# Optimization experiments

Measured on AMD Instinct MI355X. Metric: run time of the kernel, lower is better.

The kernel has to match this reference:

```python
import jax, jax.numpy as jnp
import numpy as np

N_NODES = 100000
N_EDGES = 1600000
D = 128
N_LAYERS = 3
N_GRAPHS = 64
BN_EPS = 1e-5


def setup_inputs() -> dict:
    key = jax.random.key(0)
    ks = jax.random.split(key, 8)
    x = jax.random.normal(ks[0], (N_NODES, D), dtype=jnp.float32)
    edge_index = jax.random.randint(ks[1], (2, N_EDGES), 0, N_NODES, dtype=jnp.int64)
    batch = jnp.sort(jax.random.randint(ks[2], (N_NODES,), 0, N_GRAPHS, dtype=jnp.int64))
    scale = 1.0 / np.sqrt(D)
    W1 = jax.random.normal(ks[3], (N_LAYERS, D, D), dtype=jnp.float32) * scale
    W2 = jax.random.normal(ks[4], (N_LAYERS, D, D), dtype=jnp.float32) * scale
    g1 = jnp.ones((N_LAYERS, D), dtype=jnp.float32)
    b1 = jnp.zeros((N_LAYERS, D), dtype=jnp.float32)
    g2 = jnp.ones((N_LAYERS, D), dtype=jnp.float32)
    b2 = jnp.zeros((N_LAYERS, D), dtype=jnp.float32)
    eps = jnp.zeros((N_LAYERS,), dtype=jnp.float32)
    return {"x": x, "edge_index": edge_index, "batch": batch,
            "W1": W1, "g1": g1, "b1": b1, "W2": W2, "g2": g2, "b2": b2, "eps": eps}


def _batchnorm(z, gamma, beta):
    # BatchNorm1d in training mode: biased variance over the node dimension.
    mu = jnp.mean(z, axis=0, keepdims=True)
    var = jnp.mean(jnp.square(z - mu), axis=0, keepdims=True)
    return (z - mu) * jax.lax.rsqrt(var + BN_EPS) * gamma + beta


def reference(x, edge_index, batch, W1, g1, b1, W2, g2, b2, eps):
    src, dst = edge_index[0], edge_index[1]
    h = x
    for l in range(N_LAYERS):
        # GIN aggregation: sum of neighbor features via edge-index scatter-add
        agg = jax.ops.segment_sum(h[src], dst, num_segments=N_NODES)
        z = (1.0 + eps[l]) * h + agg
        # MLP: Linear(no bias) -> BN -> ReLU -> Linear(no bias) -> BN
        z = _batchnorm(z @ W1[l], g1[l], b1[l])
        z = jax.nn.relu(z)
        z = _batchnorm(z @ W2[l], g2[l], b2[l])
        h = jax.nn.relu(z)  # gnn_non_linear
    node_emb = h
    # mean readout per graph
    counts = jax.ops.segment_sum(jnp.ones((N_NODES,), dtype=h.dtype), batch, num_segments=N_GRAPHS)
    graph_sum = jax.ops.segment_sum(h, batch, num_segments=N_GRAPHS)
    graph_emb = graph_sum / jnp.maximum(counts, 1.0)[:, None]
    # emb_normalize -> F.normalize(p=2, dim=-1)
    graph_emb = graph_emb / jnp.maximum(jnp.linalg.norm(graph_emb, axis=-1, keepdims=True), 1e-12)
    return node_emb, graph_emb
```

## Files before the change

### kernel.cpp

```cpp
#include <hip/hip_runtime.h>

#define N_NODES 100000
#define N_EDGES 1600000
#define D 128
#define N_GRAPHS 64
#define BN_EPS 1e-5f
#define NSLICE 16

#define BNODES 256
#define NBUCK ((N_NODES + BNODES - 1) / BNODES)
#define EPB 8192
#define NABLK ((N_EDGES + EPB - 1) / EPB)

typedef short short8 __attribute__((ext_vector_type(8)));
typedef float f32x4 __attribute__((ext_vector_type(4)));

__device__ inline unsigned short f2bf(float f) {
  unsigned int u = __float_as_uint(f);
  u += 0x7fffu + ((u >> 16) & 1);
  return (unsigned short)(u >> 16);
}
__device__ inline float bf2f(unsigned short h) {
  return __uint_as_float(((unsigned int)h) << 16);
}
__device__ inline void unpack8(uint4 u, float* f) {
  f[0] = __uint_as_float(u.x << 16); f[1] = __uint_as_float(u.x & 0xffff0000u);
  f[2] = __uint_as_float(u.y << 16); f[3] = __uint_as_float(u.y & 0xffff0000u);
  f[4] = __uint_as_float(u.z << 16); f[5] = __uint_as_float(u.z & 0xffff0000u);
  f[6] = __uint_as_float(u.w << 16); f[7] = __uint_as_float(u.w & 0xffff0000u);
}
__device__ inline uint4 pack8(const float* f) {
  uint4 u;
  u.x = f2bf(f[0]) | ((unsigned)f2bf(f[1]) << 16);
  u.y = f2bf(f[2]) | ((unsigned)f2bf(f[3]) << 16);
  u.z = f2bf(f[4]) | ((unsigned)f2bf(f[5]) << 16);
  u.w = f2bf(f[6]) | ((unsigned)f2bf(f[7]) << 16);
  return u;
}

__global__ __launch_bounds__(256) void k_cast(const float* __restrict__ in,
                                              unsigned short* __restrict__ o) {
  long i = ((long)blockIdx.x * blockDim.x + threadIdx.x) * 8;
  if (i >= (long)N_NODES * D) return;
  float4 a = *(const float4*)(in + i);
  float4 b = *(const float4*)(in + i + 4);
  float f[8] = {a.x, a.y, a.z, a.w, b.x, b.y, b.z, b.w};
  *(uint4*)(o + i) = pack8(f);
}

__global__ __launch_bounds__(128) void k_wprep(const float* __restrict__ W1,
                                               const float* __restrict__ W2,
                                               unsigned short* __restrict__ Wt) {
  int m = blockIdx.x;
  int n = blockIdx.y;
  int k = threadIdx.x;
  int l = m >> 1, s = m & 1;
  const float* W = (s == 0 ? W1 : W2) + (size_t)l * D * D;
  Wt[((size_t)m * D + n) * D + k] = f2bf(W[(size_t)k * D + n]);
}

__global__ __launch_bounds__(256) void k_histb(const int* __restrict__ dst,
                                               int* __restrict__ ecount) {
  __shared__ int lh[NBUCK];
  const int t = threadIdx.x;
  const int e0 = blockIdx.x * EPB;
  const int e1 = min(e0 + EPB, N_EDGES);
  for (int i = t; i < NBUCK; i += 256) lh[i] = 0;
  __syncthreads();
  for (int e = e0 + t; e < e1; e += 256) atomicAdd(&lh[dst[e] >> 8], 1);
  __syncthreads();
  for (int i = t; i < NBUCK; i += 256)
    if (lh[i]) atomicAdd(&ecount[i], lh[i]);
}

__global__ __launch_bounds__(512) void k_scanb(const int* __restrict__ ecount,
                                               int* __restrict__ ebase,
                                               int* __restrict__ gcur) {
  __shared__ int ls[512];
  int t = threadIdx.x;
  int v = (t < NBUCK) ? ecount[t] : 0;
  ls[t] = v;
  __syncthreads();
  for (int o = 1; o < 512; o <<= 1) {
    int u = (t >= o) ? ls[t - o] : 0;
    __syncthreads();
    ls[t] += u;
    __syncthreads();
  }
  int ex = ls[t] - v;
  if (t < NBUCK) { ebase[t] = ex; gcur[t] = ex; }
  if (t == 0) ebase[NBUCK] = N_EDGES;
}

__global__ __launch_bounds__(256) void k_scatA(const int* __restrict__ ei,
                                               int* __restrict__ gcur,
                                               int2* __restrict__ pairs) {
  __shared__ int lh[NBUCK];
  __shared__ int lbase[NBUCK];
  const int t = threadIdx.x;
  const int e0 = blockIdx.x * EPB;
  const int e1 = min(e0 + EPB, N_EDGES);
  for (int i = t; i < NBUCK; i += 256) lh[i] = 0;
  __syncthreads();
  for (int e = e0 + t; e < e1; e += 256) atomicAdd(&lh[ei[N_EDGES + e] >> 8], 1);
  __syncthreads();
  for (int i = t; i < NBUCK; i += 256)
    lbase[i] = (lh[i] > 0) ? atomicAdd(&gcur[i], lh[i]) : 0;
  __syncthreads();
  for (int e = e0 + t; e < e1; e += 256) {
    int s = ei[e];
    int d = ei[N_EDGES + e];
    int p = atomicAdd(&lbase[d >> 8], 1);
    pairs[p] = make_int2(s, d);
  }
}

__global__ __launch_bounds__(256) void k_scatB(const int2* __restrict__ pairs,
                                               const int* __restrict__ ebase,
                                               int* __restrict__ off,
                                               int* __restrict__ esrc) {
  __shared__ int lcnt[BNODES];
  __shared__ int ls[256];
  const int t = threadIdx.x;
  const int b = blockIdx.x;
  const int nb0 = b * BNODES;
  const int nn = min(BNODES, N_NODES - nb0);
  const int s0 = ebase[b], s1 = ebase[b + 1];
  if (t < nn) lcnt[t] = 0;
  __syncthreads();
  for (int e = s0 + t; e < s1; e += 256) atomicAdd(&lcnt[pairs[e].y - nb0], 1);
  __syncthreads();
  int c0 = (t < nn) ? lcnt[t] : 0;
  ls[t] = c0;
  __syncthreads();
  for (int o = 1; o < 256; o <<= 1) {
    int u = (t >= o) ? ls[t - o] : 0;
    __syncthreads();
    ls[t] += u;
    __syncthreads();
  }
  int pre = ls[t] - c0;
  if (t < nn) {
    off[nb0 + t] = s0 + pre;
    lcnt[t] = s0 + pre;
  }
  __syncthreads();
  for (int e = s0 + t; e < s1; e += 256) {
    int2 p = pairs[e];
    int pos = atomicAdd(&lcnt[p.y - nb0], 1);
    esrc[pos] = p.x;
  }
  if (b == 0 && t == 0) off[N_NODES] = N_EDGES;
}

template <int MODE>
__global__ __launch_bounds__(256) void k_aggz(const unsigned short* __restrict__ h,
                                              const int* __restrict__ off,
                                              const int* __restrict__ esrc,
                                              const float* __restrict__ epsp,
                                              const float* __restrict__ sc,
                                              const float* __restrict__ tb,
                                              unsigned short* __restrict__ z) {
  const int lane = threadIdx.x & 63;
  const int n = blockIdx.x * 4 + (threadIdx.x >> 6);
  const int c = lane << 1;
  float S0 = 0.f, S1 = 0.f, T0 = 0.f, T1 = 0.f;
  if (MODE == 1) { S0 = sc[c]; S1 = sc[c + 1]; T0 = tb[c]; T1 = tb[c + 1]; }
  const float e = 1.0f + epsp[0];
  const int o0 = off[n], o1 = off[n + 1];

  float a0, a1;
  {
    unsigned int u = *(const unsigned int*)(h + (size_t)n * D + c);
    float lo = __uint_as_float(u << 16);
    float hi = __uint_as_float(u & 0xffff0000u);
    if (MODE == 1) {
      lo = fmaxf(fmaf(lo, S0, T0), 0.f);
      hi = fmaxf(fmaf(hi, S1, T1), 0.f);
    }
    a0 = e * lo;
    a1 = e * hi;
  }

  int j = o0;
  for (; j + 7 < o1; j += 8) {
    int i0 = esrc[j], i1 = esrc[j + 1], i2 = esrc[j + 2], i3 = esrc[j + 3];
    int i4 = esrc[j + 4], i5 = esrc[j + 5], i6 = esrc[j + 6], i7 = esrc[j + 7];
    unsigned int u0 = *(const unsigned int*)(h + (size_t)i0 * D + c);
    unsigned int u1 = *(const unsigned int*)(h + (size_t)i1 * D + c);
    unsigned int u2 = *(const unsigned int*)(h + (size_t)i2 * D + c);
    unsigned int u3 = *(const unsigned int*)(h + (size_t)i3 * D + c);
    unsigned int u4 = *(const unsigned int*)(h + (size_t)i4 * D + c);
    unsigned int u5 = *(const unsigned int*)(h + (size_t)i5 * D + c);
    unsigned int u6 = *(const unsigned int*)(h + (size_t)i6 * D + c);
    unsigned int u7 = *(const unsigned int*)(h + (size_t)i7 * D + c);
    float l0 = __uint_as_float(u0 << 16), h0 = __uint_as_float(u0 & 0xffff0000u);
    float l1 = __uint_as_float(u1 << 16), h1 = __uint_as_float(u1 & 0xffff0000u);
    float l2 = __uint_as_float(u2 << 16), h2 = __uint_as_float(u2 & 0xffff0000u);
    float l3 = __uint_as_float(u3 << 16), h3 = __uint_as_float(u3 & 0xffff0000u);
    float l4 = __uint_as_float(u4 << 16), h4 = __uint_as_float(u4 & 0xffff0000u);
    float l5 = __uint_as_float(u5 << 16), h5 = __uint_as_float(u5 & 0xffff0000u);
    float l6 = __uint_as_float(u6 << 16), h6 = __uint_as_float(u6 & 0xffff0000u);
    float l7 = __uint_as_float(u7 << 16), h7 = __uint_as_float(u7 & 0xffff0000u);
    if (MODE == 1) {
      l0 = fmaxf(fmaf(l0, S0, T0), 0.f); h0 = fmaxf(fmaf(h0, S1, T1), 0.f);
      l1 = fmaxf(fmaf(l1, S0, T0), 0.f); h1 = fmaxf(fmaf(h1, S1, T1), 0.f);
      l2 = fmaxf(fmaf(l2, S0, T0), 0.f); h2 = fmaxf(fmaf(h2, S1, T1), 0.f);
      l3 = fmaxf(fmaf(l3, S0, T0), 0.f); h3 = fmaxf(fmaf(h3, S1, T1), 0.f);
      l4 = fmaxf(fmaf(l4, S0, T0), 0.f); h4 = fmaxf(fmaf(h4, S1, T1), 0.f);
      l5 = fmaxf(fmaf(l5, S0, T0), 0.f); h5 = fmaxf(fmaf(h5, S1, T1), 0.f);
      l6 = fmaxf(fmaf(l6, S0, T0), 0.f); h6 = fmaxf(fmaf(h6, S1, T1), 0.f);
      l7 = fmaxf(fmaf(l7, S0, T0), 0.f); h7 = fmaxf(fmaf(h7, S1, T1), 0.f);
    }
    a0 += ((l0 + l1) + (l2 + l3)) + ((l4 + l5) + (l6 + l7));
    a1 += ((h0 + h1) + (h2 + h3)) + ((h4 + h5) + (h6 + h7));
  }
  for (; j + 3 < o1; j += 4) {
    int i0 = esrc[j], i1 = esrc[j + 1], i2 = esrc[j + 2], i3 = esrc[j + 3];
    unsigned int u0 = *(const unsigned int*)(h + (size_t)i0 * D + c);
    unsigned int u1 = *(const unsigned int*)(h + (size_t)i1 * D + c);
    unsigned int u2 = *(const unsigned int*)(h + (size_t)i2 * D + c);
    unsigned int u3 = *(const unsigned int*)(h + (size_t)i3 * D + c);
    float l0 = __uint_as_float(u0 << 16), h0 = __uint_as_float(u0 & 0xffff0000u);
    float l1 = __uint_as_float(u1 << 16), h1 = __uint_as_float(u1 & 0xffff0000u);
    float l2 = __uint_as_float(u2 << 16), h2 = __uint_as_float(u2 & 0xffff0000u);
    float l3 = __uint_as_float(u3 << 16), h3 = __uint_as_float(u3 & 0xffff0000u);
    if (MODE == 1) {
      l0 = fmaxf(fmaf(l0, S0, T0), 0.f); h0 = fmaxf(fmaf(h0, S1, T1), 0.f);
      l1 = fmaxf(fmaf(l1, S0, T0), 0.f); h1 = fmaxf(fmaf(h1, S1, T1), 0.f);
      l2 = fmaxf(fmaf(l2, S0, T0), 0.f); h2 = fmaxf(fmaf(h2, S1, T1), 0.f);
      l3 = fmaxf(fmaf(l3, S0, T0), 0.f); h3 = fmaxf(fmaf(h3, S1, T1), 0.f);
    }
    a0 += (l0 + l1) + (l2 + l3);
    a1 += (h0 + h1) + (h2 + h3);
  }
  for (; j < o1; j++) {
    unsigned int u0 = *(const unsigned int*)(h + (size_t)esrc[j] * D + c);
    float l0 = __uint_as_float(u0 << 16), h0 = __uint_as_float(u0 & 0xffff0000u);
    if (MODE == 1) {
      l0 = fmaxf(fmaf(l0, S0, T0), 0.f);
      h0 = fmaxf(fmaf(h0, S1, T1), 0.f);
    }
    a0 += l0;
    a1 += h0;
  }
  unsigned int pk = (unsigned int)f2bf(a0) | ((unsigned int)f2bf(a1) << 16);
  *(unsigned int*)(z + (size_t)n * D + c) = pk;
}

template <int MODE>
__global__ __launch_bounds__(256) void k_gemm(const unsigned short* __restrict__ A,
                                              const unsigned short* __restrict__ Wt,
                                              unsigned short* __restrict__ out,
                                              const float* __restrict__ psA,
                                              const float* __restrict__ pqA,
                                              const float* __restrict__ gamA,
                                              const float* __restrict__ betA,
                                              float* __restrict__ ssum,
                                              float* __restrict__ ssq) {
  __shared__ unsigned short Zs[64 * 136];
  __shared__ float psumL[4 * 128];
  __shared__ float psqL[4 * 128];
  __shared__ float scL[128];
  __shared__ float tbL[128];
  const int t = threadIdx.x;
  const int row0 = blockIdx.x * 64;

  if constexpr (MODE == 1) {
    if (t < 128) {
      float S = 0.f, Q = 0.f;
#pragma unroll
      for (int i = 0; i < NSLICE; i++) { S += psA[i * 128 + t]; Q += pqA[i * 128 + t]; }
      float m = S * (1.0f / (float)N_NODES);
      float v = Q * (1.0f / (float)N_NODES) - m * m;
      float r = rsqrtf(v + BN_EPS);
      float s = r * gamA[t];
      scL[t] = s;
      tbL[t] = betA[t] - m * s;
    }
    __syncthreads();
  }

#pragma unroll
  for (int i = 0; i < 4; i++) {
    int q = t + i * 256;
    int r = q >> 4, cb = (q & 15) << 3;
    int grow = row0 + r;
    uint4 u = make_uint4(0u, 0u, 0u, 0u);
    if (grow < N_NODES) {
      u = *(const uint4*)(A + (size_t)grow * D + cb);
      if constexpr (MODE == 1) {
        float f[8];
        unpack8(u, f);
#pragma unroll
        for (int jj = 0; jj < 8; jj++)
          f[jj] = fmaxf(fmaf(f[jj], scL[cb + jj], tbL[cb + jj]), 0.f);
        u = pack8(f);
      }
    }
    *(uint4*)&Zs[r * 136 + cb] = u;
  }
  __syncthreads();

  const int lane = t & 63;
  const int wave = t >> 6;
  const int quad = lane >> 4;
  const int lr = lane & 15;
  const int m0 = wave * 16;

  f32x4 acc[8];
#pragma unroll
  for (int i = 0; i < 8; i++) acc[i] = (f32x4){0.f, 0.f, 0.f, 0.f};

#pragma unroll
  for (int kc = 0; kc < 128; kc += 32) {
    short8 af = *(const short8*)&Zs[(m0 + lr) * 136 + kc + quad * 8];
#pragma unroll
    for (int nt = 0; nt < 8; nt++) {
      short8 bf = *(const short8*)(Wt + (size_t)(nt * 16 + lr) * D + kc + quad * 8);
      acc[nt] = __builtin_amdgcn_mfma_f32_16x16x32_bf16(af, bf, acc[nt], 0, 0, 0);
    }
  }

#pragma unroll
  for (int nt = 0; nt < 8; nt++) {
    float s = acc[nt][0] + acc[nt][1] + acc[nt][2] + acc[nt][3];
    float qq = acc[nt][0] * acc[nt][0] + acc[nt][1] * acc[nt][1] +
               acc[nt][2] * acc[nt][2] + acc[nt][3] * acc[nt][3];
    s += __shfl_xor(s, 16);
    s += __shfl_xor(s, 32);
    qq += __shfl_xor(qq, 16);
    qq += __shfl_xor(qq, 32);
    if (quad == 0) {
      psumL[wave * 128 + nt * 16 + lr] = s;
      psqL[wave * 128 + nt * 16 + lr] = qq;
    }
  }

#pragma unroll
  for (int rr = 0; rr < 4; rr++) {
    int grow = row0 + m0 + quad * 4 + rr;
    if (grow < N_NODES) {
#pragma unroll
      for (int nt = 0; nt < 8; nt++)
        out[(size_t)grow * D + nt * 16 + lr] = f2bf(acc[nt][rr]);
    }
  }

  __syncthreads();
  if (t < 128) {
    float S = psumL[t] + psumL[128 + t] + psumL[256 + t] + psumL[384 + t];
    float Q = psqL[t] + psqL[128 + t] + psqL[256 + t] + psqL[384 + t];
    int slice = blockIdx.x & (NSLICE - 1);
    atomicAdd(&ssum[slice * 128 + t], S);
    atomicAdd(&ssq[slice * 128 + t], Q);
  }
}

__global__ void k_bnfin(const float* __restrict__ ssum, const float* __restrict__ ssq,
                        const float* __restrict__ gamma, const float* __restrict__ beta,
                        float* __restrict__ sc, float* __restrict__ tb) {
  int f = threadIdx.x;
  float S = 0.f, Q = 0.f;
  for (int i = 0; i < NSLICE; i++) { S += ssum[i * 128 + f]; Q += ssq[i * 128 + f]; }
  float m = S * (1.0f / (float)N_NODES);
  float v = Q * (1.0f / (float)N_NODES) - m * m;
  float r = rsqrtf(v + BN_EPS);
  float s = r * gamma[f];
  sc[f] = s;
  tb[f] = beta[f] - m * s;
}

#define RCH 64
__global__ __launch_bounds__(128) void k_readout(const unsigned short* __restrict__ y,
                                                 const int* __restrict__ batch,
                                                 const float* __restrict__ psA,
                                                 const float* __restrict__ pqA,
                                                 const float* __restrict__ gam,
                                                 const float* __restrict__ bet,
                                                 float* __restrict__ node_out,
                                                 float* __restrict__ gsum,
                                                 int* __restrict__ gcnt) {
  int start = blockIdx.x * RCH;
  int end = min(start + RCH, N_NODES);
  if (start >= end) return;
  int f = threadIdx.x;
  float S = 0.f, Q = 0.f;
#pragma unroll
  for (int i = 0; i < NSLICE; i++) { S += psA[i * 128 + f]; Q += pqA[i * 128 + f]; }
  float m = S * (1.0f / (float)N_NODES);
  float v = Q * (1.0f / (float)N_NODES) - m * m;
  float r = rsqrtf(v + BN_EPS);
  float s = r * gam[f];
  float tt = bet[f] - m * s;

  float acc = 0.f;
  int cnt = 0;
  int curg = batch[start];
  for (int n = start; n < end; n++) {
    int gg = batch[n];
    float vv = fmaxf(fmaf(bf2f(y[(size_t)n * D + f]), s, tt), 0.f);
    node_out[(size_t)n * D + f] = vv;
    if (gg != curg) {
      atomicAdd(&gsum[curg * D + f], acc);
      if (f == 0) atomicAdd(&gcnt[curg], cnt);
      acc = 0.f; cnt = 0; curg = gg;
    }
    acc += vv;
    cnt++;
  }
  atomicAdd(&gsum[curg * D + f], acc);
  if (f == 0) atomicAdd(&gcnt[curg], cnt);
}

__global__ __launch_bounds__(128) void k_gnorm(const float* __restrict__ gsum,
                                               const int* __restrict__ gcnt,
                                               float* __restrict__ out) {
  __shared__ float red[128];
  int g = blockIdx.x, f = threadIdx.x;
  float c = (float)gcnt[g];
  float v = gsum[g * D + f] / fmaxf(c, 1.0f);
  red[f] = v * v;
  __syncthreads();
  for (int o = 64; o > 0; o >>= 1) {
    if (f < o) red[f] += red[f + o];
    __syncthreads();
  }
  float nrm = sqrtf(red[0]);
  out[(size_t)g * D + f] = v / fmaxf(nrm, 1e-12f);
}

extern "C" void kernel_launch(void* const* d_in, const int* in_sizes, int n_in,
                              void* d_out, int out_size, void* d_ws, size_t ws_size,
                              hipStream_t stream) {
  const float* x   = (const float*)d_in[0];
  const int*   ei  = (const int*)d_in[1];
  const int*   bat = (const int*)d_in[2];
  const float* W1  = (const float*)d_in[3];
  const float* g1  = (const float*)d_in[4];
  const float* b1  = (const float*)d_in[5];
  const float* W2  = (const float*)d_in[6];
  const float* g2  = (const float*)d_in[7];
  const float* b2  = (const float*)d_in[8];
  const float* eps = (const float*)d_in[9];
  float* out = (float*)d_out;

  char* w = (char*)d_ws;
  const size_t FEAT_B = (size_t)N_NODES * D * 2;
  unsigned short* xb   = (unsigned short*)w; w += FEAT_B;
  unsigned short* bufA = (unsigned short*)w; w += FEAT_B;
  unsigned short* bufB = (unsigned short*)w; w += FEAT_B;
  unsigned short* bufC = (unsigned short*)w; w += FEAT_B;
  unsigned short* WtB  = (unsigned short*)w; w += (size_t)6 * D * D * 2;
  int* off   = (int*)w; w += 400016;
  int* ebase = (int*)w; w += 2048;
  int* gcur  = (int*)w; w += 2048;
  int* esrc  = (int*)w; w += (size_t)N_EDGES * 4;
  float* sc2 = (float*)w; w += 512;
  float* tb2 = (float*)w; w += 512;
  char* zreg = w;
  int* ecount  = (int*)w; w += 2048;
  float* stats = (float*)w; w += (size_t)6 * 2 * NSLICE * 128 * 4;
  float* gsum  = (float*)w; w += (size_t)N_GRAPHS * D * 4;
  int* gcnt    = (int*)w; w += 256;
  size_t zbytes = (size_t)((char*)w - zreg);
  int2* pairs = (int2*)bufA;

  hipMemsetAsync(zreg, 0, zbytes, stream);

  k_cast<<<(N_NODES * D / 8 + 255) / 256, 256, 0, stream>>>(x, xb);
  k_wprep<<<dim3(6, 128), 128, 0, stream>>>(W1, W2, WtB);

  k_histb<<<NABLK, 256, 0, stream>>>(ei + N_EDGES, ecount);
  k_scanb<<<1, 512, 0, stream>>>(ecount, ebase, gcur);
  k_scatA<<<NABLK, 256, 0, stream>>>(ei, gcur, pairs);
  k_scatB<<<NBUCK, 256, 0, stream>>>(pairs, ebase, off, esrc);

  const int gemm_grid = (N_NODES + 63) / 64;
  const int aggz_grid = N_NODES / 4;

  for (int l = 0; l < 3; l++) {
    float* s1 = stats + (size_t)(l * 2 + 0) * 2 * NSLICE * 128;
    float* q1 = s1 + NSLICE * 128;
    float* s2 = stats + (size_t)(l * 2 + 1) * 2 * NSLICE * 128;
    float* q2 = s2 + NSLICE * 128;
    const unsigned short* Wa = WtB + (size_t)(l * 2 + 0) * D * D;
    const unsigned short* Wb = WtB + (size_t)(l * 2 + 1) * D * D;
    if (l == 0) {
      k_aggz<0><<<aggz_grid, 256, 0, stream>>>(xb, off, esrc, eps + l,
                                               nullptr, nullptr, bufA);
    } else {
      k_aggz<1><<<aggz_grid, 256, 0, stream>>>(bufC, off, esrc, eps + l,
                                               sc2, tb2, bufA);
    }
    k_gemm<0><<<gemm_grid, 256, 0, stream>>>(bufA, Wa, bufB,
                                             nullptr, nullptr, nullptr, nullptr,
                                             s1, q1);
    k_gemm<1><<<gemm_grid, 256, 0, stream>>>(bufB, Wb, bufC,
                                             s1, q1, g1 + (size_t)l * D, b1 + (size_t)l * D,
                                             s2, q2);
    if (l < 2) {
      k_bnfin<<<1, 128, 0, stream>>>(s2, q2, g2 + (size_t)l * D, b2 + (size_t)l * D,
                                     sc2, tb2);
    }
  }

  float* ps2f = stats + (size_t)(2 * 2 + 1) * 2 * NSLICE * 128;
  float* pq2f = ps2f + NSLICE * 128;
  k_readout<<<(N_NODES + RCH - 1) / RCH, 128, 0, stream>>>(
      bufC, bat, ps2f, pq2f, g2 + (size_t)2 * D, b2 + (size_t)2 * D,
      out, gsum, gcnt);
  k_gnorm<<<N_GRAPHS, 128, 0, stream>>>(gsum, gcnt, out + (size_t)N_NODES * D);
}
```

Baseline: 644.5 us.

## Split neighbor gather across half-waves with 8-byte loads and fuse BN finalize

```diff
diff --git a/kernel.cpp b/kernel.cpp
--- a/kernel.cpp
+++ b/kernel.cpp
@@ -148,7 +148,7 @@
   for (int e = s0 + t; e < s1; e += 256) {
     int2 p = pairs[e];
     int pos = atomicAdd(&lcnt[p.y - nb0], 1);
-    esrc[pos] = p.x;
+    esrc[pos] = p.x << 8;
   }
   if (b == 0 && t == 0) off[N_NODES] = N_EDGES;
 }
@@ -156,96 +156,99 @@
 template <int MODE>
 __global__ __launch_bounds__(256) void k_aggz(const unsigned short* __restrict__ h,
                                               const int* __restrict__ off,
-                                              const int* __restrict__ esrc,
+                                              const int* __restrict__ esrcB,
                                               const float* __restrict__ epsp,
                                               const float* __restrict__ sc,
                                               const float* __restrict__ tb,
                                               unsigned short* __restrict__ z) {
   const int lane = threadIdx.x & 63;
   const int n = blockIdx.x * 4 + (threadIdx.x >> 6);
-  const int c = lane << 1;
-  float S0 = 0.f, S1 = 0.f, T0 = 0.f, T1 = 0.f;
-  if (MODE == 1) { S0 = sc[c]; S1 = sc[c + 1]; T0 = tb[c]; T1 = tb[c + 1]; }
+  const int half = lane >> 5;
+  const int hl = lane & 31;
+  const int c = hl << 2;
+  const char* hb = (const char*)h;
+  const int cb = hl << 3;
+
+  float S0 = 0.f, S1 = 0.f, S2 = 0.f, S3 = 0.f;
+  float T0 = 0.f, T1 = 0.f, T2 = 0.f, T3 = 0.f;
+  if (MODE == 1) {
+    float4 s4 = *(const float4*)(sc + c);
+    float4 t4 = *(const float4*)(tb + c);
+    S0 = s4.x; S1 = s4.y; S2 = s4.z; S3 = s4.w;
+    T0 = t4.x; T1 = t4.y; T2 = t4.z; T3 = t4.w;
+  }
   const float e = 1.0f + epsp[0];
   const int o0 = off[n], o1 = off[n + 1];
 
-  float a0, a1;
+  float a0, a1, a2, a3;
   {
-    unsigned int u = *(const unsigned int*)(h + (size_t)n * D + c);
-    float lo = __uint_as_float(u << 16);
-    float hi = __uint_as_float(u & 0xffff0000u);
+    uint2 u = *(const uint2*)(hb + (size_t)n * 256 + cb);
+    float v0 = __uint_as_float(u.x << 16), v1 = __uint_as_float(u.x & 0xffff0000u);
+    float v2 = __uint_as_float(u.y << 16), v3 = __uint_as_float(u.y & 0xffff0000u);
     if (MODE == 1) {
-      lo = fmaxf(fmaf(lo, S0, T0), 0.f);
-      hi = fmaxf(fmaf(hi, S1, T1), 0.f);
-    }
-    a0 = e * lo;
-    a1 = e * hi;
+      v0 = fmaxf(fmaf(v0, S0, T0), 0.f); v1 = fmaxf(fmaf(v1, S1, T1), 0.f);
+      v2 = fmaxf(fmaf(v2, S2, T2), 0.f); v3 = fmaxf(fmaf(v3, S3, T3), 0.f);
+    }
+    float ee = (half == 0) ? e : 0.f;
+    a0 = ee * v0; a1 = ee * v1; a2 = ee * v2; a3 = ee * v3;
   }
 
   int j = o0;
   for (; j + 7 < o1; j += 8) {
-    int i0 = esrc[j], i1 = esrc[j + 1], i2 = esrc[j + 2], i3 = esrc[j + 3];
-    int i4 = esrc[j + 4], i5 = esrc[j + 5], i6 = esrc[j + 6], i7 = esrc[j + 7];
-    unsigned int u0 = *(const unsigned int*)(h + (size_t)i0 * D + c);
-    unsigned int u1 = *(const unsigned int*)(h + (size_t)i1 * D + c);
-    unsigned int u2 = *(const unsigned int*)(h + (size_t)i2 * D + c);
-    unsigned int u3 = *(const unsigned int*)(h + (size_t)i3 * D + c);
-    unsigned int u4 = *(const unsigned int*)(h + (size_t)i4 * D + c);
-    unsigned int u5 = *(const unsigned int*)(h + (size_t)i5 * D + c);
-    unsigned int u6 = *(const unsigned int*)(h + (size_t)i6 * D + c);
-    unsigned int u7 = *(const unsigned int*)(h + (size_t)i7 * D + c);
-    float l0 = __uint_as_float(u0 << 16), h0 = __uint_as_float(u0 & 0xffff0000u);
-    float l1 = __uint_as_float(u1 << 16), h1 = __uint_as_float(u1 & 0xffff0000u);
-    float l2 = __uint_as_float(u2 << 16), h2 = __uint_as_float(u2 & 0xffff0000u);
-    float l3 = __uint_as_float(u3 << 16), h3 = __uint_as_float(u3 & 0xffff0000u);
-    float l4 = __uint_as_float(u4 << 16), h4 = __uint_as_float(u4 & 0xffff0000u);
-    float l5 = __uint_as_float(u5 << 16), h5 = __uint_as_float(u5 & 0xffff0000u);
-    float l6 = __uint_as_float(u6 << 16), h6 = __uint_as_float(u6 & 0xffff0000u);
-    float l7 = __uint_as_float(u7 << 16), h7 = __uint_as_float(u7 & 0xffff0000u);
+    int b0 = esrcB[j + half];
+    int b1 = esrcB[j + 2 + half];
+    int b2 = esrcB[j + 4 + half];
+    int b3 = esrcB[j + 6 + half];
+    uint2 u0 = *(const uint2*)(hb + (unsigned)b0 + cb);
+    uint2 u1 = *(const uint2*)(hb + (unsigned)b1 + cb);
+    uint2 u2 = *(const uint2*)(hb + (unsigned)b2 + cb);
+    uint2 u3 = *(const uint2*)(hb + (unsigned)b3 + cb);
+    float p0 = __uint_as_float(u0.x << 16), p1 = __uint_as_float(u0.x & 0xffff0000u);
+    float p2 = __uint_as_float(u0.y << 16), p3 = __uint_as_float(u0.y & 0xffff0000u);
+    float q0 = __uint_as_float(u1.x << 16), q1 = __uint_as_float(u1.x & 0xffff0000u);
+    float q2 = __uint_as_float(u1.y << 16), q3 = __uint_as_float(u1.y & 0xffff0000u);
+    float r0 = __uint_as_float(u2.x << 16), r1 = __uint_as_float(u2.x & 0xffff0000u);
+    float r2 = __uint_as_float(u2.y << 16), r3 = __uint_as_float(u2.y & 0xffff0000u);
+    float s0 = __uint_as_float(u3.x << 16), s1 = __uint_as_float(u3.x & 0xffff0000u);
+    float s2 = __uint_as_float(u3.y << 16), s3 = __uint_as_float(u3.y & 0xffff0000u);
     if (MODE == 1) {
-      l0 = fmaxf(fmaf(l0, S0, T0), 0.f); h0 = fmaxf(fmaf(h0, S1, T1), 0.f);
-      l1 = fmaxf(fmaf(l1, S0, T0), 0.f); h1 = fmaxf(fmaf(h1, S1, T1), 0.f);
-      l2 = fmaxf(fmaf(l2, S0, T0), 0.f); h2 = fmaxf(fmaf(h2, S1, T1), 0.f);
-      l3 = fmaxf(fmaf(l3, S0, T0), 0.f); h3 = fmaxf(fmaf(h3, S1, T1), 0.f);
-      l4 = fmaxf(fmaf(l4, S0, T0), 0.f); h4 = fmaxf(fmaf(h4, S1, T1), 0.f);
-      l5 = fmaxf(fmaf(l5, S0, T0), 0.f); h5 = fmaxf(fmaf(h5, S1, T1), 0.f);
-      l6 = fmaxf(fmaf(l6, S0, T0), 0.f); h6 = fmaxf(fmaf(h6, S1, T1), 0.f);
-      l7 = fmaxf(fmaf(l7, S0, T0), 0.f); h7 = fmaxf(fmaf(h7, S1, T1), 0.f);
-    }
-    a0 += ((l0 + l1) + (l2 + l3)) + ((l4 + l5) + (l6 + l7));
-    a1 += ((h0 + h1) + (h2 + h3)) + ((h4 + h5) + (h6 + h7));
-  }
-  for (; j + 3 < o1; j += 4) {
-    int i0 = esrc[j], i1 = esrc[j + 1], i2 = esrc[j + 2], i3 = esrc[j + 3];
-    unsigned int u0 = *(const unsigned int*)(h + (size_t)i0 * D + c);
-    unsigned int u1 = *(const unsigned int*)(h + (size_t)i1 * D + c);
-    unsigned int u2 = *(const unsigned int*)(h + (size_t)i2 * D + c);
-    unsigned int u3 = *(const unsigned int*)(h + (size_t)i3 * D + c);
-    float l0 = __uint_as_float(u0 << 16), h0 = __uint_as_float(u0 & 0xffff0000u);
-    float l1 = __uint_as_float(u1 << 16), h1 = __uint_as_float(u1 & 0xffff0000u);
-    float l2 = __uint_as_float(u2 << 16), h2 = __uint_as_float(u2 & 0xffff0000u);
-    float l3 = __uint_as_float(u3 << 16), h3 = __uint_as_float(u3 & 0xffff0000u);
-    if (MODE == 1) {
-      l0 = fmaxf(fmaf(l0, S0, T0), 0.f); h0 = fmaxf(fmaf(h0, S1, T1), 0.f);
-      l1 = fmaxf(fmaf(l1, S0, T0), 0.f); h1 = fmaxf(fmaf(h1, S1, T1), 0.f);
-      l2 = fmaxf(fmaf(l2, S0, T0), 0.f); h2 = fmaxf(fmaf(h2, S1, T1), 0.f);
-      l3 = fmaxf(fmaf(l3, S0, T0), 0.f); h3 = fmaxf(fmaf(h3, S1, T1), 0.f);
-    }
-    a0 += (l0 + l1) + (l2 + l3);
-    a1 += (h0 + h1) + (h2 + h3);
-  }
-  for (; j < o1; j++) {
-    unsigned int u0 = *(const unsigned int*)(h + (size_t)esrc[j] * D + c);
-    float l0 = __uint_as_float(u0 << 16), h0 = __uint_as_float(u0 & 0xffff0000u);
-    if (MODE == 1) {
-      l0 = fmaxf(fmaf(l0, S0, T0), 0.f);
-      h0 = fmaxf(fmaf(h0, S1, T1), 0.f);
-    }
-    a0 += l0;
-    a1 += h0;
-  }
-  unsigned int pk = (unsigned int)f2bf(a0) | ((unsigned int)f2bf(a1) << 16);
-  *(unsigned int*)(z + (size_t)n * D + c) = pk;
+      p0 = fmaxf(fmaf(p0, S0, T0), 0.f); p1 = fmaxf(fmaf(p1, S1, T1), 0.f);
+      p2 = fmaxf(fmaf(p2, S2, T2), 0.f); p3 = fmaxf(fmaf(p3, S3, T3), 0.f);
+      q0 = fmaxf(fmaf(q0, S0, T0), 0.f); q1 = fmaxf(fmaf(q1, S1, T1), 0.f);
+      q2 = fmaxf(fmaf(q2, S2, T2), 0.f); q3 = fmaxf(fmaf(q3, S3, T3), 0.f);
+      r0 = fmaxf(fmaf(r0, S0, T0), 0.f); r1 = fmaxf(fmaf(r1, S1, T1), 0.f);
+      r2 = fmaxf(fmaf(r2, S2, T2), 0.f); r3 = fmaxf(fmaf(r3, S3, T3), 0.f);
+      s0 = fmaxf(fmaf(s0, S0, T0), 0.f); s1 = fmaxf(fmaf(s1, S1, T1), 0.f);
+      s2 = fmaxf(fmaf(s2, S2, T2), 0.f); s3 = fmaxf(fmaf(s3, S3, T3), 0.f);
+    }
+    a0 += (p0 + q0) + (r0 + s0);
+    a1 += (p1 + q1) + (r1 + s1);
+    a2 += (p2 + q2) + (r2 + s2);
+    a3 += (p3 + q3) + (r3 + s3);
+  }
+  for (; j < o1; j += 2) {
+    if (j + half < o1) {
+      int b0 = esrcB[j + half];
+      uint2 u0 = *(const uint2*)(hb + (unsigned)b0 + cb);
+      float p0 = __uint_as_float(u0.x << 16), p1 = __uint_as_float(u0.x & 0xffff0000u);
+      float p2 = __uint_as_float(u0.y << 16), p3 = __uint_as_float(u0.y & 0xffff0000u);
+      if (MODE == 1) {
+        p0 = fmaxf(fmaf(p0, S0, T0), 0.f); p1 = fmaxf(fmaf(p1, S1, T1), 0.f);
+        p2 = fmaxf(fmaf(p2, S2, T2), 0.f); p3 = fmaxf(fmaf(p3, S3, T3), 0.f);
+      }
+      a0 += p0; a1 += p1; a2 += p2; a3 += p3;
+    }
+  }
+
+  a0 += __shfl_xor(a0, 32);
+  a1 += __shfl_xor(a1, 32);
+  a2 += __shfl_xor(a2, 32);
+  a3 += __shfl_xor(a3, 32);
+  if (half == 0) {
+    unsigned int w0 = (unsigned int)f2bf(a0) | ((unsigned int)f2bf(a1) << 16);
+    unsigned int w1 = (unsigned int)f2bf(a2) | ((unsigned int)f2bf(a3) << 16);
+    *(uint2*)((char*)z + (size_t)n * 256 + cb) = make_uint2(w0, w1);
+  }
 }
 
 template <int MODE>
@@ -257,12 +260,18 @@
                                               const float* __restrict__ gamA,
                                               const float* __restrict__ betA,
                                               float* __restrict__ ssum,
-                                              float* __restrict__ ssq) {
+                                              float* __restrict__ ssq,
+                                              const float* __restrict__ gamO,
+                                              const float* __restrict__ betO,
+                                              float* __restrict__ sc2o,
+                                              float* __restrict__ tb2o,
+                                              int* __restrict__ dctr) {
   __shared__ unsigned short Zs[64 * 136];
   __shared__ float psumL[4 * 128];
   __shared__ float psqL[4 * 128];
   __shared__ float scL[128];
   __shared__ float tbL[128];
+  __shared__ int lastFlag;
   const int t = threadIdx.x;
   const int row0 = blockIdx.x * 64;
 
@@ -355,20 +364,32 @@
     atomicAdd(&ssum[slice * 128 + t], S);
     atomicAdd(&ssq[slice * 128 + t], Q);
   }
-}
-
-__global__ void k_bnfin(const float* __restrict__ ssum, const float* __restrict__ ssq,
-                        const float* __restrict__ gamma, const float* __restrict__ beta,
-                        float* __restrict__ sc, float* __restrict__ tb) {
-  int f = threadIdx.x;
-  float S = 0.f, Q = 0.f;
-  for (int i = 0; i < NSLICE; i++) { S += ssum[i * 128 + f]; Q += ssq[i * 128 + f]; }
-  float m = S * (1.0f / (float)N_NODES);
-  float v = Q * (1.0f / (float)N_NODES) - m * m;
-  float r = rsqrtf(v + BN_EPS);
-  float s = r * gamma[f];
-  sc[f] = s;
-  tb[f] = beta[f] - m * s;
+
+  if (sc2o != nullptr) {
+    __threadfence();
+    __syncthreads();
+    if (t == 0) {
+      int v = atomicAdd(dctr, 1);
+      lastFlag = (v == (int)gridDim.x - 1) ? 1 : 0;
+    }
+    __syncthreads();
+    if (lastFlag && t < 128) {
+      float S = 0.f, Q = 0.f;
+#pragma unroll
+      for (int i = 0; i < NSLICE; i++) {
+        S += __hip_atomic_load(&ssum[i * 128 + t], __ATOMIC_RELAXED,
+                               __HIP_MEMORY_SCOPE_AGENT);
+        Q += __hip_atomic_load(&ssq[i * 128 + t], __ATOMIC_RELAXED,
+                               __HIP_MEMORY_SCOPE_AGENT);
+      }
+      float m = S * (1.0f / (float)N_NODES);
+      float v = Q * (1.0f / (float)N_NODES) - m * m;
+      float r = rsqrtf(v + BN_EPS);
+      float s = r * gamO[t];
+      sc2o[t] = s;
+      tb2o[t] = betO[t] - m * s;
+    }
+  }
 }
 
 #define RCH 64
@@ -463,6 +484,7 @@
   float* stats = (float*)w; w += (size_t)6 * 2 * NSLICE * 128 * 4;
   float* gsum  = (float*)w; w += (size_t)N_GRAPHS * D * 4;
   int* gcnt    = (int*)w; w += 256;
+  int* dctr    = (int*)w; w += 256;
   size_t zbytes = (size_t)((char*)w - zreg);
   int2* pairs = (int2*)bufA;
 
@@ -495,13 +517,21 @@
     }
     k_gemm<0><<<gemm_grid, 256, 0, stream>>>(bufA, Wa, bufB,
                                              nullptr, nullptr, nullptr, nullptr,
-                                             s1, q1);
-    k_gemm<1><<<gemm_grid, 256, 0, stream>>>(bufB, Wb, bufC,
-                                             s1, q1, g1 + (size_t)l * D, b1 + (size_t)l * D,
-                                             s2, q2);
+                                             s1, q1,
+                                             nullptr, nullptr, nullptr, nullptr,
+                                             nullptr);
     if (l < 2) {
-      k_bnfin<<<1, 128, 0, stream>>>(s2, q2, g2 + (size_t)l * D, b2 + (size_t)l * D,
-                                     sc2, tb2);
+      k_gemm<1><<<gemm_grid, 256, 0, stream>>>(bufB, Wb, bufC,
+                                               s1, q1, g1 + (size_t)l * D, b1 + (size_t)l * D,
+                                               s2, q2,
+                                               g2 + (size_t)l * D, b2 + (size_t)l * D,
+                                               sc2, tb2, dctr + l);
+    } else {
+      k_gemm<1><<<gemm_grid, 256, 0, stream>>>(bufB, Wb, bufC,
+                                               s1, q1, g1 + (size_t)l * D, b1 + (size_t)l * D,
+                                               s2, q2,
+                                               nullptr, nullptr, nullptr, nullptr,
+                                               nullptr);
     }
   }
 
```

Result: slower. 1.029 ms (+59.7%).

## Pre-scale edge sources to byte offsets, stage W in LDS, drop BN stat reduction

Applied to the files above, without the earlier changes.

```diff
diff --git a/kernel.cpp b/kernel.cpp
--- a/kernel.cpp
+++ b/kernel.cpp
@@ -148,7 +148,7 @@
   for (int e = s0 + t; e < s1; e += 256) {
     int2 p = pairs[e];
     int pos = atomicAdd(&lcnt[p.y - nb0], 1);
-    esrc[pos] = p.x;
+    esrc[pos] = p.x << 8;
   }
   if (b == 0 && t == 0) off[N_NODES] = N_EDGES;
 }
@@ -156,7 +156,7 @@
 template <int MODE>
 __global__ __launch_bounds__(256) void k_aggz(const unsigned short* __restrict__ h,
                                               const int* __restrict__ off,
-                                              const int* __restrict__ esrc,
+                                              const int* __restrict__ esrcB,
                                               const float* __restrict__ epsp,
                                               const float* __restrict__ sc,
                                               const float* __restrict__ tb,
@@ -164,6 +164,8 @@
   const int lane = threadIdx.x & 63;
   const int n = blockIdx.x * 4 + (threadIdx.x >> 6);
   const int c = lane << 1;
+  const int cb = lane << 2;
+  const char* hb = (const char*)h;
   float S0 = 0.f, S1 = 0.f, T0 = 0.f, T1 = 0.f;
   if (MODE == 1) { S0 = sc[c]; S1 = sc[c + 1]; T0 = tb[c]; T1 = tb[c + 1]; }
   const float e = 1.0f + epsp[0];
@@ -171,7 +173,7 @@
 
   float a0, a1;
   {
-    unsigned int u = *(const unsigned int*)(h + (size_t)n * D + c);
+    unsigned int u = *(const unsigned int*)(hb + (size_t)n * 256 + cb);
     float lo = __uint_as_float(u << 16);
     float hi = __uint_as_float(u & 0xffff0000u);
     if (MODE == 1) {
@@ -184,16 +186,16 @@
 
   int j = o0;
   for (; j + 7 < o1; j += 8) {
-    int i0 = esrc[j], i1 = esrc[j + 1], i2 = esrc[j + 2], i3 = esrc[j + 3];
-    int i4 = esrc[j + 4], i5 = esrc[j + 5], i6 = esrc[j + 6], i7 = esrc[j + 7];
-    unsigned int u0 = *(const unsigned int*)(h + (size_t)i0 * D + c);
-    unsigned int u1 = *(const unsigned int*)(h + (size_t)i1 * D + c);
-    unsigned int u2 = *(const unsigned int*)(h + (size_t)i2 * D + c);
-    unsigned int u3 = *(const unsigned int*)(h + (size_t)i3 * D + c);
-    unsigned int u4 = *(const unsigned int*)(h + (size_t)i4 * D + c);
-    unsigned int u5 = *(const unsigned int*)(h + (size_t)i5 * D + c);
-    unsigned int u6 = *(const unsigned int*)(h + (size_t)i6 * D + c);
-    unsigned int u7 = *(const unsigned int*)(h + (size_t)i7 * D + c);
+    int b0 = esrcB[j], b1 = esrcB[j + 1], b2 = esrcB[j + 2], b3 = esrcB[j + 3];
+    int b4 = esrcB[j + 4], b5 = esrcB[j + 5], b6 = esrcB[j + 6], b7 = esrcB[j + 7];
+    unsigned int u0 = *(const unsigned int*)(hb + (unsigned)b0 + cb);
+    unsigned int u1 = *(const unsigned int*)(hb + (unsigned)b1 + cb);
+    unsigned int u2 = *(const unsigned int*)(hb + (unsigned)b2 + cb);
+    unsigned int u3 = *(const unsigned int*)(hb + (unsigned)b3 + cb);
+    unsigned int u4 = *(const unsigned int*)(hb + (unsigned)b4 + cb);
+    unsigned int u5 = *(const unsigned int*)(hb + (unsigned)b5 + cb);
+    unsigned int u6 = *(const unsigned int*)(hb + (unsigned)b6 + cb);
+    unsigned int u7 = *(const unsigned int*)(hb + (unsigned)b7 + cb);
     float l0 = __uint_as_float(u0 << 16), h0 = __uint_as_float(u0 & 0xffff0000u);
     float l1 = __uint_as_float(u1 << 16), h1 = __uint_as_float(u1 & 0xffff0000u);
     float l2 = __uint_as_float(u2 << 16), h2 = __uint_as_float(u2 & 0xffff0000u);
@@ -216,11 +218,11 @@
     a1 += ((h0 + h1) + (h2 + h3)) + ((h4 + h5) + (h6 + h7));
   }
   for (; j + 3 < o1; j += 4) {
-    int i0 = esrc[j], i1 = esrc[j + 1], i2 = esrc[j + 2], i3 = esrc[j + 3];
-    unsigned int u0 = *(const unsigned int*)(h + (size_t)i0 * D + c);
-    unsigned int u1 = *(const unsigned int*)(h + (size_t)i1 * D + c);
-    unsigned int u2 = *(const unsigned int*)(h + (size_t)i2 * D + c);
-    unsigned int u3 = *(const unsigned int*)(h + (size_t)i3 * D + c);
+    int b0 = esrcB[j], b1 = esrcB[j + 1], b2 = esrcB[j + 2], b3 = esrcB[j + 3];
+    unsigned int u0 = *(const unsigned int*)(hb + (unsigned)b0 + cb);
+    unsigned int u1 = *(const unsigned int*)(hb + (unsigned)b1 + cb);
+    unsigned int u2 = *(const unsigned int*)(hb + (unsigned)b2 + cb);
+    unsigned int u3 = *(const unsigned int*)(hb + (unsigned)b3 + cb);
     float l0 = __uint_as_float(u0 << 16), h0 = __uint_as_float(u0 & 0xffff0000u);
     float l1 = __uint_as_float(u1 << 16), h1 = __uint_as_float(u1 & 0xffff0000u);
     float l2 = __uint_as_float(u2 << 16), h2 = __uint_as_float(u2 & 0xffff0000u);
@@ -235,7 +237,7 @@
     a1 += (h0 + h1) + (h2 + h3);
   }
   for (; j < o1; j++) {
-    unsigned int u0 = *(const unsigned int*)(h + (size_t)esrc[j] * D + c);
+    unsigned int u0 = *(const unsigned int*)(hb + (unsigned)esrcB[j] + cb);
     float l0 = __uint_as_float(u0 << 16), h0 = __uint_as_float(u0 & 0xffff0000u);
     if (MODE == 1) {
       l0 = fmaxf(fmaf(l0, S0, T0), 0.f);
@@ -245,7 +247,7 @@
     a1 += h0;
   }
   unsigned int pk = (unsigned int)f2bf(a0) | ((unsigned int)f2bf(a1) << 16);
-  *(unsigned int*)(z + (size_t)n * D + c) = pk;
+  *(unsigned int*)((char*)z + (size_t)n * 256 + cb) = pk;
 }
 
 template <int MODE>
@@ -259,12 +261,18 @@
                                               float* __restrict__ ssum,
                                               float* __restrict__ ssq) {
   __shared__ unsigned short Zs[64 * 136];
-  __shared__ float psumL[4 * 128];
-  __shared__ float psqL[4 * 128];
+  __shared__ unsigned short Ws[128 * 136];
   __shared__ float scL[128];
   __shared__ float tbL[128];
   const int t = threadIdx.x;
   const int row0 = blockIdx.x * 64;
+
+#pragma unroll
+  for (int i = 0; i < 8; i++) {
+    int q = t + i * 256;
+    int r = q >> 4, cbw = (q & 15) << 3;
+    *(uint4*)&Ws[r * 136 + cbw] = *(const uint4*)(Wt + (size_t)r * D + cbw);
+  }
 
   if constexpr (MODE == 1) {
     if (t < 128) {
@@ -317,11 +325,12 @@
     short8 af = *(const short8*)&Zs[(m0 + lr) * 136 + kc + quad * 8];
 #pragma unroll
     for (int nt = 0; nt < 8; nt++) {
-      short8 bf = *(const short8*)(Wt + (size_t)(nt * 16 + lr) * D + kc + quad * 8);
+      short8 bf = *(const short8*)&Ws[(nt * 16 + lr) * 136 + kc + quad * 8];
       acc[nt] = __builtin_amdgcn_mfma_f32_16x16x32_bf16(af, bf, acc[nt], 0, 0, 0);
     }
   }
 
+  const int slice = blockIdx.x & (NSLICE - 1);
 #pragma unroll
   for (int nt = 0; nt < 8; nt++) {
     float s = acc[nt][0] + acc[nt][1] + acc[nt][2] + acc[nt][3];
@@ -332,8 +341,8 @@
     qq += __shfl_xor(qq, 16);
     qq += __shfl_xor(qq, 32);
     if (quad == 0) {
-      psumL[wave * 128 + nt * 16 + lr] = s;
-      psqL[wave * 128 + nt * 16 + lr] = qq;
+      atomicAdd(&ssum[slice * 128 + nt * 16 + lr], s);
+      atomicAdd(&ssq[slice * 128 + nt * 16 + lr], qq);
     }
   }
 
@@ -345,15 +354,6 @@
       for (int nt = 0; nt < 8; nt++)
         out[(size_t)grow * D + nt * 16 + lr] = f2bf(acc[nt][rr]);
     }
-  }
-
-  __syncthreads();
-  if (t < 128) {
-    float S = psumL[t] + psumL[128 + t] + psumL[256 + t] + psumL[384 + t];
-    float Q = psqL[t] + psqL[128 + t] + psqL[256 + t] + psqL[384 + t];
-    int slice = blockIdx.x & (NSLICE - 1);
-    atomicAdd(&ssum[slice * 128 + t], S);
-    atomicAdd(&ssq[slice * 128 + t], Q);
   }
 }
 
```

After: 617.7 us. 4.2% less time.
